# Kernel tuning notes

Hardware: AMD Instinct MI355X
Metric: run time of the kernel (lower is better)

Reference implementation:

```python
import jax, jax.numpy as jnp
import numpy as np

N_NODES = 100000
N_EDGES = 3200000
D_FEAT = 64
ALPHA = 0.1
K_STEPS = 10


def setup_inputs() -> dict:
    key = jax.random.key(0)
    k1, k2, k3, k4 = jax.random.split(key, 4)
    x = jax.random.normal(k1, (N_NODES, D_FEAT), dtype=jnp.float32)
    edge_row = jax.random.randint(k2, (N_EDGES,), 0, N_NODES, dtype=jnp.int32)
    edge_col = jax.random.randint(k3, (N_EDGES,), 0, N_NODES, dtype=jnp.int32)
    edge_weight = jax.random.uniform(k4, (N_EDGES,), dtype=jnp.float32)
    return {"x": x, "edge_row": edge_row, "edge_col": edge_col, "edge_weight": edge_weight}


def reference(x, edge_row, edge_col, edge_weight):
    # APPNP propagation: h <- (1-alpha) * A @ h + alpha * x, repeated K times.
    # A is sparse [N, N] given as an edge list; A @ h done via gather + segment_sum.
    def spmm(h):
        msgs = edge_weight[:, None] * h[edge_col]          # [E, d]
        return jax.ops.segment_sum(msgs, edge_row, num_segments=N_NODES)  # [N, d]

    h = x
    for _ in range(K_STEPS):
        h = (1.0 - ALPHA) * spmm(h) + ALPHA * x
    return h
```

## Files before the change

### kernel.cpp

```cpp
#include <hip/hip_runtime.h>

typedef unsigned int u32;
typedef unsigned long long u64;
typedef unsigned char u8;
typedef u32   v4u __attribute__((ext_vector_type(4)));
typedef float v4f __attribute__((ext_vector_type(4)));

#define NN 100000
#define NE 3200000
#define DF 64
#define ALPHA 0.1f
#define BETA 0.9f
#define K_STEPS 10
#define NBKT 782
#define SLOTS 4608
#define EPT 16
#define CHUNK (256 * EPT)
#define NCHB ((NE + CHUNK - 1) / CHUNK)

__device__ __forceinline__ u32 rne_bf16(float f) {
    u32 u = __float_as_uint(f);
    return (u + 0x7FFFu + ((u >> 16) & 1u)) >> 16;
}
__device__ __forceinline__ float bf_lo(u32 w) { return __uint_as_float(w << 16); }
__device__ __forceinline__ float bf_hi(u32 w) { return __uint_as_float(w & 0xFFFF0000u); }

__global__ void init_cur(int* __restrict__ bcur) {
    int i = blockIdx.x * 256 + threadIdx.x;
    if (i < NBKT) bcur[i] = i * SLOTS;
}

__global__ void bucket_scatter(const int* __restrict__ row, const int* __restrict__ col,
                               const float* __restrict__ w, int* __restrict__ bcur,
                               u32* __restrict__ edgesT, u8* __restrict__ lr) {
    __shared__ int scnt[NBKT];
    __shared__ int sbase[NBKT];
    for (int i = threadIdx.x; i < NBKT; i += 256) scnt[i] = 0;
    __syncthreads();
    int base = blockIdx.x * CHUNK + threadIdx.x;
    int rows[EPT];
    #pragma unroll
    for (int j = 0; j < EPT; ++j) {
        int e = base + j * 256;
        int r = (e < NE) ? row[e] : -1;
        rows[j] = r;
        if (r >= 0) atomicAdd(&scnt[r >> 7], 1);
    }
    __syncthreads();
    for (int i = threadIdx.x; i < NBKT; i += 256) {
        int c = scnt[i];
        sbase[i] = c ? atomicAdd(&bcur[i], c) : 0;
    }
    __syncthreads();
    for (int i = threadIdx.x; i < NBKT; i += 256) scnt[i] = 0;
    __syncthreads();
    #pragma unroll
    for (int j = 0; j < EPT; ++j) {
        int e = base + j * 256;
        int r = rows[j];
        if (r >= 0) {
            int b = r >> 7;
            int rank = atomicAdd(&scnt[b], 1);
            int pos = sbase[b] + rank;
            if (pos < (b + 1) * SLOTS) {
                edgesT[pos] = ((u32)col[e] << 15) | (rne_bf16(w[e]) & 0x7FFFu);
                lr[pos] = (u8)(r & 127);
            }
        }
    }
}

__global__ void scan_buckets(const int* __restrict__ bcur, int* __restrict__ bbase) {
    __shared__ int s[1024];
    int i = threadIdx.x;
    int v = 0;
    if (i < NBKT) {
        v = bcur[i] - i * SLOTS;
        if (v > SLOTS) v = SLOTS;
    }
    s[i] = v;
    __syncthreads();
    for (int off = 1; off < 1024; off <<= 1) {
        int t = (i >= off) ? s[i - off] : 0;
        __syncthreads();
        s[i] += t;
        __syncthreads();
    }
    if (i < NBKT) bbase[i] = s[i] - v;
}

__global__ void build_rows(const u32* __restrict__ edgesT, const u8* __restrict__ lr,
                           const int* __restrict__ bcur, const int* __restrict__ bbase,
                           u32* __restrict__ edgesF, int* __restrict__ rp) {
    __shared__ int rc[128];
    __shared__ int rb[128];
    int b = blockIdx.x;
    int cnt = bcur[b] - b * SLOTS;
    if (cnt > SLOTS) cnt = SLOTS;
    int base = bbase[b];
    int tbase = b * SLOTS;
    if (threadIdx.x < 128) rc[threadIdx.x] = 0;
    __syncthreads();
    for (int e = threadIdx.x; e < cnt; e += 256)
        atomicAdd(&rc[lr[tbase + e]], 1);
    __syncthreads();
    if (threadIdx.x < 128) rb[threadIdx.x] = rc[threadIdx.x];
    __syncthreads();
    for (int off = 1; off < 128; off <<= 1) {
        int t = (threadIdx.x < 128 && threadIdx.x >= off) ? rb[threadIdx.x - off] : 0;
        __syncthreads();
        if (threadIdx.x < 128) rb[threadIdx.x] += t;
        __syncthreads();
    }
    if (threadIdx.x < 128) {
        int r = b * 128 + threadIdx.x;
        if (r < NN) rp[r] = base + rb[threadIdx.x];
        rc[threadIdx.x] = rb[threadIdx.x] - rc[threadIdx.x];
    }
    __syncthreads();
    for (int e = threadIdx.x; e < cnt; e += 256) {
        int pos = atomicAdd(&rc[lr[tbase + e]], 1);
        edgesF[base + pos] = edgesT[tbase + e];
    }
}

__global__ void conv_x(const float* __restrict__ x, u32* __restrict__ xb) {
    int t = blockIdx.x * blockDim.x + threadIdx.x;
    if (t >= NN * 8) return;
    const float4* src = (const float4*)(x + (size_t)t * 8);
    float4 a = src[0], b = src[1];
    uint4 o;
    o.x = rne_bf16(a.x) | (rne_bf16(a.y) << 16);
    o.y = rne_bf16(a.z) | (rne_bf16(a.w) << 16);
    o.z = rne_bf16(b.x) | (rne_bf16(b.y) << 16);
    o.w = rne_bf16(b.z) | (rne_bf16(b.w) << 16);
    *(uint4*)(xb + (size_t)t * 4) = o;
}

__global__ __launch_bounds__(256) void
gather_step(const int* __restrict__ rp, const u32* __restrict__ edges,
            const u32* __restrict__ h, const u32* __restrict__ xb,
            u32* __restrict__ hn, float* __restrict__ outf, int final_step) {
    int lane = threadIdx.x & 63;
    int node = blockIdx.x * 4 + (threadIdx.x >> 6);
    int slice = lane >> 3;
    int fg = lane & 7;

    int start = (node == 0) ? 0 : rp[node - 1];
    int end = rp[node];

    float a0=0.f,a1=0.f,a2=0.f,a3=0.f,a4=0.f,a5=0.f,a6=0.f,a7=0.f;
    #pragma unroll 2
    for (int e = start + slice; e < end; e += 8) {
        u32 ew = __builtin_nontemporal_load(edges + e);
        u32 c = ew >> 15;
        float wv = __uint_as_float((ew & 0x7FFFu) << 16);
        const uint4 hv = *(const uint4*)(h + ((size_t)c << 5) + (fg << 2));
        a0 += wv * bf_lo(hv.x); a1 += wv * bf_hi(hv.x);
        a2 += wv * bf_lo(hv.y); a3 += wv * bf_hi(hv.y);
        a4 += wv * bf_lo(hv.z); a5 += wv * bf_hi(hv.z);
        a6 += wv * bf_lo(hv.w); a7 += wv * bf_hi(hv.w);
    }
    for (int m = 8; m <= 32; m <<= 1) {
        a0 += __shfl_xor(a0, m, 64); a1 += __shfl_xor(a1, m, 64);
        a2 += __shfl_xor(a2, m, 64); a3 += __shfl_xor(a3, m, 64);
        a4 += __shfl_xor(a4, m, 64); a5 += __shfl_xor(a5, m, 64);
        a6 += __shfl_xor(a6, m, 64); a7 += __shfl_xor(a7, m, 64);
    }
    uint4 xv = *(const uint4*)(xb + ((size_t)node << 5) + (fg << 2));
    float o0 = BETA * a0 + ALPHA * bf_lo(xv.x);
    float o1 = BETA * a1 + ALPHA * bf_hi(xv.x);
    float o2 = BETA * a2 + ALPHA * bf_lo(xv.y);
    float o3 = BETA * a3 + ALPHA * bf_hi(xv.y);
    float o4 = BETA * a4 + ALPHA * bf_lo(xv.z);
    float o5 = BETA * a5 + ALPHA * bf_hi(xv.z);
    float o6 = BETA * a6 + ALPHA * bf_lo(xv.w);
    float o7 = BETA * a7 + ALPHA * bf_hi(xv.w);

    if (!final_step) {
        if (slice == 0) {
            v4u o;
            o.x = rne_bf16(o0) | (rne_bf16(o1) << 16);
            o.y = rne_bf16(o2) | (rne_bf16(o3) << 16);
            o.z = rne_bf16(o4) | (rne_bf16(o5) << 16);
            o.w = rne_bf16(o6) | (rne_bf16(o7) << 16);
            __builtin_nontemporal_store(o, (v4u*)(hn + ((size_t)node << 5) + (fg << 2)));
        }
    } else {
        if (slice < 2) {
            v4f v;
            if (slice) { v.x = o4; v.y = o5; v.z = o6; v.w = o7; }
            else       { v.x = o0; v.y = o1; v.z = o2; v.w = o3; }
            __builtin_nontemporal_store(v, (v4f*)(outf + (size_t)node * DF + fg * 8 + slice * 4));
        }
    }
}


extern "C" void kernel_launch(void* const* d_in, const int* in_sizes, int n_in,
                              void* d_out, int out_size, void* d_ws, size_t ws_size,
                              hipStream_t stream) {
    const float* x    = (const float*)d_in[0];
    const int*   erow = (const int*)  d_in[1];
    const int*   ecol = (const int*)  d_in[2];
    const float* ew   = (const float*)d_in[3];
    float* out = (float*)d_out;

    char* ws = (char*)d_ws;
    u32* edgesF = (u32*)(ws);
    u32* xb     = (u32*)(ws + 12800000);
    u32* hA     = (u32*)(ws + 25600000);
    u32* hB     = (u32*)(ws + 38400000);
    u32* edgesT = (u32*)(ws + 25600000);
    u8*  lr     = (u8*) (ws + 40100000);
    int* rp     = (int*)(ws + 51200000);
    int* bcur   = (int*)(ws + 51600000);
    int* bbase  = (int*)(ws + 51604096);

    dim3 blk(256);
    dim3 gChunk(NCHB);
    dim3 gConv((NN * 8 + 255) / 256);
    dim3 gG(NN / 4);

    init_cur<<<dim3((NBKT + 255) / 256), blk, 0, stream>>>(bcur);
    bucket_scatter<<<gChunk, blk, 0, stream>>>(erow, ecol, ew, bcur, edgesT, lr);
    scan_buckets<<<1, 1024, 0, stream>>>(bcur, bbase);
    build_rows<<<NBKT, blk, 0, stream>>>(edgesT, lr, bcur, bbase, edgesF, rp);
    conv_x<<<gConv, blk, 0, stream>>>(x, xb);

    for (int k = 0; k < K_STEPS; ++k) {
        const u32* src = (k == 0) ? xb : ((k & 1) ? hA : hB);
        u32* dst = (k & 1) ? hB : hA;
        int fin = (k == K_STEPS - 1);
        gather_step<<<gG, blk, 0, stream>>>(rp, edgesF, src, xb,
                                            fin ? nullptr : dst,
                                            fin ? out : nullptr, fin);
    }
}
```

Baseline: 895.2 us.

## Reuse atomic ranks in bucketing and keep entries in registers when building CSR

Bucket scatter now keeps the shared-memory atomic rank from the counting pass. This drops the second atomic pass and its extra sync. Column, weight and local row are packed into a single 64-bit entry. build_rows uses 512 threads, loads each entry once into registers, takes its in-row rank from one atomic, and writes output without a second read and atomic pass. The cost is more register pressure (EPT 32, nine cached entries per thread) and a larger temporary buffer that overlaps the x/h workspace.

```diff
diff --git a/kernel.cpp b/kernel.cpp
--- a/kernel.cpp
+++ b/kernel.cpp
@@ -2,7 +2,6 @@
 
 typedef unsigned int u32;
 typedef unsigned long long u64;
-typedef unsigned char u8;
 typedef u32   v4u __attribute__((ext_vector_type(4)));
 typedef float v4f __attribute__((ext_vector_type(4)));
 
@@ -14,9 +13,10 @@
 #define K_STEPS 10
 #define NBKT 782
 #define SLOTS 4608
-#define EPT 16
+#define EPT 32
 #define CHUNK (256 * EPT)
 #define NCHB ((NE + CHUNK - 1) / CHUNK)
+#define BRT 512
 
 __device__ __forceinline__ u32 rne_bf16(float f) {
     u32 u = __float_as_uint(f);
@@ -32,19 +32,17 @@
 
 __global__ void bucket_scatter(const int* __restrict__ row, const int* __restrict__ col,
                                const float* __restrict__ w, int* __restrict__ bcur,
-                               u32* __restrict__ edgesT, u8* __restrict__ lr) {
+                               u64* __restrict__ e64) {
     __shared__ int scnt[NBKT];
     __shared__ int sbase[NBKT];
     for (int i = threadIdx.x; i < NBKT; i += 256) scnt[i] = 0;
     __syncthreads();
     int base = blockIdx.x * CHUNK + threadIdx.x;
-    int rows[EPT];
+    int rank[EPT];
     #pragma unroll
     for (int j = 0; j < EPT; ++j) {
         int e = base + j * 256;
-        int r = (e < NE) ? row[e] : -1;
-        rows[j] = r;
-        if (r >= 0) atomicAdd(&scnt[r >> 7], 1);
+        rank[j] = (e < NE) ? atomicAdd(&scnt[row[e] >> 7], 1) : 0;
     }
     __syncthreads();
     for (int i = threadIdx.x; i < NBKT; i += 256) {
@@ -52,19 +50,16 @@
         sbase[i] = c ? atomicAdd(&bcur[i], c) : 0;
     }
     __syncthreads();
-    for (int i = threadIdx.x; i < NBKT; i += 256) scnt[i] = 0;
-    __syncthreads();
     #pragma unroll
     for (int j = 0; j < EPT; ++j) {
         int e = base + j * 256;
-        int r = rows[j];
-        if (r >= 0) {
+        if (e < NE) {
+            int r = row[e];
             int b = r >> 7;
-            int rank = atomicAdd(&scnt[b], 1);
-            int pos = sbase[b] + rank;
+            int pos = sbase[b] + rank[j];
             if (pos < (b + 1) * SLOTS) {
-                edgesT[pos] = ((u32)col[e] << 15) | (rne_bf16(w[e]) & 0x7FFFu);
-                lr[pos] = (u8)(r & 127);
+                u32 cw = ((u32)col[e] << 15) | (rne_bf16(w[e]) & 0x7FFFu);
+                e64[pos] = ((u64)(r & 127) << 32) | cw;
             }
         }
     }
@@ -89,22 +84,32 @@
     if (i < NBKT) bbase[i] = s[i] - v;
 }
 
-__global__ void build_rows(const u32* __restrict__ edgesT, const u8* __restrict__ lr,
-                           const int* __restrict__ bcur, const int* __restrict__ bbase,
-                           u32* __restrict__ edgesF, int* __restrict__ rp) {
+__global__ __launch_bounds__(BRT) void
+build_rows(const u64* __restrict__ e64, const int* __restrict__ bcur,
+           const int* __restrict__ bbase, u32* __restrict__ edgesF,
+           int* __restrict__ rp) {
     __shared__ int rc[128];
     __shared__ int rb[128];
     int b = blockIdx.x;
     int cnt = bcur[b] - b * SLOTS;
     if (cnt > SLOTS) cnt = SLOTS;
     int base = bbase[b];
-    int tbase = b * SLOTS;
+    const u64* src = e64 + (size_t)b * SLOTS;
     if (threadIdx.x < 128) rc[threadIdx.x] = 0;
     __syncthreads();
-    for (int e = threadIdx.x; e < cnt; e += 256)
-        atomicAdd(&rc[lr[tbase + e]], 1);
-    __syncthreads();
-    if (threadIdx.x < 128) rb[threadIdx.x] = rc[threadIdx.x];
+    u64 ent[9];
+    int rk[9];
+    #pragma unroll
+    for (int it = 0; it < 9; ++it) {
+        int e = threadIdx.x + it * BRT;
+        if (e < cnt) {
+            ent[it] = src[e];
+            rk[it] = atomicAdd(&rc[(int)(ent[it] >> 32)], 1);
+        }
+    }
+    __syncthreads();
+    int myc = (threadIdx.x < 128) ? rc[threadIdx.x] : 0;
+    if (threadIdx.x < 128) rb[threadIdx.x] = myc;
     __syncthreads();
     for (int off = 1; off < 128; off <<= 1) {
         int t = (threadIdx.x < 128 && threadIdx.x >= off) ? rb[threadIdx.x - off] : 0;
@@ -115,12 +120,14 @@
     if (threadIdx.x < 128) {
         int r = b * 128 + threadIdx.x;
         if (r < NN) rp[r] = base + rb[threadIdx.x];
-        rc[threadIdx.x] = rb[threadIdx.x] - rc[threadIdx.x];
-    }
-    __syncthreads();
-    for (int e = threadIdx.x; e < cnt; e += 256) {
-        int pos = atomicAdd(&rc[lr[tbase + e]], 1);
-        edgesF[base + pos] = edgesT[tbase + e];
+        rc[threadIdx.x] = rb[threadIdx.x] - myc;
+    }
+    __syncthreads();
+    #pragma unroll
+    for (int it = 0; it < 9; ++it) {
+        int e = threadIdx.x + it * BRT;
+        if (e < cnt)
+            edgesF[base + rc[(int)(ent[it] >> 32)] + rk[it]] = (u32)ent[it];
     }
 }
 
@@ -211,8 +218,7 @@
     u32* xb     = (u32*)(ws + 12800000);
     u32* hA     = (u32*)(ws + 25600000);
     u32* hB     = (u32*)(ws + 38400000);
-    u32* edgesT = (u32*)(ws + 25600000);
-    u8*  lr     = (u8*) (ws + 40100000);
+    u64* e64    = (u64*)(ws + 12800000);
     int* rp     = (int*)(ws + 51200000);
     int* bcur   = (int*)(ws + 51600000);
     int* bbase  = (int*)(ws + 51604096);
@@ -223,9 +229,9 @@
     dim3 gG(NN / 4);
 
     init_cur<<<dim3((NBKT + 255) / 256), blk, 0, stream>>>(bcur);
-    bucket_scatter<<<gChunk, blk, 0, stream>>>(erow, ecol, ew, bcur, edgesT, lr);
+    bucket_scatter<<<gChunk, blk, 0, stream>>>(erow, ecol, ew, bcur, e64);
     scan_buckets<<<1, 1024, 0, stream>>>(bcur, bbase);
-    build_rows<<<NBKT, blk, 0, stream>>>(edgesT, lr, bcur, bbase, edgesF, rp);
+    build_rows<<<NBKT, dim3(BRT), 0, stream>>>(e64, bcur, bbase, edgesF, rp);
     conv_x<<<gConv, blk, 0, stream>>>(x, xb);
 
     for (int k = 0; k < K_STEPS; ++k) {
```

Result: faster. 825.8 us (-7.7%).
